# Kernel tuning notes

Hardware: AMD Instinct MI355X
Metric: run time of the kernel (lower is better)

The kernel has to match this reference:

```python
import jax, jax.numpy as jnp
import numpy as np

N_NODES = 1_000_000
HID = 64
BATCH = 262_144


def _gru_cell(x, h, w_ih, w_hh, b_ih, b_hh):
    # PyTorch GRUCell semantics. w_ih/w_hh: [3H, H]; gate order r, z, n.
    gi = x @ w_ih.T + b_ih
    gh = h @ w_hh.T + b_hh
    i_r, i_z, i_n = jnp.split(gi, 3, axis=-1)
    h_r, h_z, h_n = jnp.split(gh, 3, axis=-1)
    r = jax.nn.sigmoid(i_r + h_r)
    z = jax.nn.sigmoid(i_z + h_z)
    n = jnp.tanh(i_n + r * h_n)
    return (1.0 - z) * n + z * h


def setup_inputs() -> dict:
    key = jax.random.key(0)
    ks = jax.random.split(key, 16)
    H = HID
    s = lambda fan_in: 1.0 / np.sqrt(fan_in)
    return {
        "node_pairs": jax.random.randint(ks[0], (BATCH, 2), 0, N_NODES, dtype=jnp.int64)
        if jax.config.jax_enable_x64 else jax.random.randint(ks[0], (BATCH, 2), 0, N_NODES, dtype=jnp.int32),
        "memory": jax.random.normal(ks[1], (N_NODES, H), dtype=jnp.float32),
        "msg_w1": jax.random.uniform(ks[2], (H, 2 * H), jnp.float32, -s(2 * H), s(2 * H)),
        "msg_b1": jax.random.uniform(ks[3], (H,), jnp.float32, -s(2 * H), s(2 * H)),
        "msg_w2": jax.random.uniform(ks[4], (H, H), jnp.float32, -s(H), s(H)),
        "msg_b2": jax.random.uniform(ks[5], (H,), jnp.float32, -s(H), s(H)),
        "gru_w_ih": jax.random.uniform(ks[6], (3 * H, H), jnp.float32, -s(H), s(H)),
        "gru_w_hh": jax.random.uniform(ks[7], (3 * H, H), jnp.float32, -s(H), s(H)),
        "gru_b_ih": jax.random.uniform(ks[8], (3 * H,), jnp.float32, -s(H), s(H)),
        "gru_b_hh": jax.random.uniform(ks[9], (3 * H,), jnp.float32, -s(H), s(H)),
        "lp_w1": jax.random.uniform(ks[10], (H, 2 * H), jnp.float32, -s(2 * H), s(2 * H)),
        "lp_b1": jax.random.uniform(ks[11], (H,), jnp.float32, -s(2 * H), s(2 * H)),
        "lp_w2": jax.random.uniform(ks[12], (1, H), jnp.float32, -s(H), s(H)),
        "lp_b2": jax.random.uniform(ks[13], (1,), jnp.float32, -s(H), s(H)),
    }


def reference(node_pairs, memory, msg_w1, msg_b1, msg_w2, msg_b2,
              gru_w_ih, gru_w_hh, gru_b_ih, gru_b_hh,
              lp_w1, lp_b1, lp_w2, lp_b2):
    n1_mem = memory[node_pairs[:, 0]]  # [B, H]
    n2_mem = memory[node_pairs[:, 1]]  # [B, H]
    x = jnp.concatenate([n1_mem, n2_mem], axis=1)  # [B, 2H]
    messages = jax.nn.relu(x @ msg_w1.T + msg_b1) @ msg_w2.T + msg_b2  # [B, H]
    n1_upd = _gru_cell(messages, n1_mem, gru_w_ih, gru_w_hh, gru_b_ih, gru_b_hh)
    n2_upd = _gru_cell(messages, n2_mem, gru_w_ih, gru_w_hh, gru_b_ih, gru_b_hh)
    combined = jnp.concatenate([n1_upd, n2_upd], axis=1)  # [B, 2H]
    h = jax.nn.relu(combined @ lp_w1.T + lp_b1)  # dropout inactive in eval
    out = jax.nn.sigmoid(h @ lp_w2.T + lp_b2)  # [B, 1]
    return out.squeeze(-1)
```

## Files before the change

### kernel.cpp

```cpp
#include <hip/hip_runtime.h>

#define BATCH 262144

typedef __attribute__((ext_vector_type(8))) short short8;
typedef __attribute__((ext_vector_type(4))) float f32x4;

static __device__ __forceinline__ unsigned cvtpk(float lo, float hi) {
    unsigned r;
    asm("v_cvt_pk_bf16_f32 %0, %1, %2" : "=v"(r) : "v"(lo), "v"(hi));
    return r;
}
static __device__ __forceinline__ float b2f(short s) {
    return __uint_as_float(((unsigned)(unsigned short)s) << 16);
}
static __device__ __forceinline__ float sigm(float x) { return 1.0f / (1.0f + __expf(-x)); }
static __device__ __forceinline__ float tanh_f(float x) { return 1.0f - 2.0f / (__expf(2.0f * x) + 1.0f); }

#define WAVE_FENCE() asm volatile("" ::: "memory")

static __device__ __forceinline__ int sw128(int row, int cb) { return row * 128 + (cb ^ ((row & 7) << 4)); }
static __device__ __forceinline__ int sw256(int row, int cb) { return row * 256 + (cb ^ ((row & 7) << 4)); }

#define WLDS_BYTES 90112
#define NCHUNK (WLDS_BYTES / 16)

__global__ __launch_bounds__(768) void tgn_kernel(
    const int* __restrict__ pairs, const float* __restrict__ memory,
    const float* __restrict__ w1g, const float* __restrict__ w2g,
    const float* __restrict__ wihg, const float* __restrict__ whhg,
    const float* __restrict__ lw1g,
    const float* __restrict__ b1, const float* __restrict__ b2,
    const float* __restrict__ bih, const float* __restrict__ bhh,
    const float* __restrict__ lb1, const float* __restrict__ lw2,
    const float* __restrict__ lb2, float* __restrict__ out)
{
    __shared__ __align__(16) char wlds[WLDS_BYTES];
    __shared__ __align__(16) char work[12][6144];

    const int tid = threadIdx.x;
    const int w  = tid >> 6;
    const int l  = tid & 63;
    const int lr = l & 15;
    const int lg = l >> 4;

    for (int c = tid; c < NCHUNK; c += 768) {
        int byte = c * 16;
        int e    = c * 8;
        const float* src;
        int base, sh;
        if (e < 8192)       { src = w1g  + e;         base = 0;     sh = 8; }
        else if (e < 12288) { src = w2g  + e - 8192;  base = 16384; sh = 7; }
        else if (e < 24576) { src = wihg + e - 12288; base = 24576; sh = 7; }
        else if (e < 36864) { src = whhg + e - 24576; base = 49152; sh = 7; }
        else                { src = lw1g + e - 36864; base = 73728; sh = 8; }
        f32x4 v0 = *(const f32x4*)src;
        f32x4 v1 = *(const f32x4*)(src + 4);
        union { unsigned u[4]; short8 s; } r;
        r.u[0] = cvtpk(v0[0], v0[1]); r.u[1] = cvtpk(v0[2], v0[3]);
        r.u[2] = cvtpk(v1[0], v1[1]); r.u[3] = cvtpk(v1[2], v1[3]);
        int t   = byte - base;
        int row = t >> sh;
        int dst = base + (t ^ ((row & 7) << 4));
        *(short8*)(wlds + dst) = r.s;
    }
    __syncthreads();

    char* n1b = &work[w][0];
    char* n2b = &work[w][2048];
    char* hmb = &work[w][4096];

    const char* w1l  = wlds + 0;
    const char* w2l  = wlds + 16384;
    const char* wihl = wlds + 24576;
    const char* whhl = wlds + 49152;
    const char* lw1l = wlds + 73728;

    const f32x4 z4 = {0.0f, 0.0f, 0.0f, 0.0f};

    const int waveid = blockIdx.x * 12 + w;

    int2 pr[4];
#pragma unroll
    for (int rr = 0; rr < 4; ++rr)
        pr[rr] = *(const int2*)(pairs + (waveid * 16 + rr * 4 + lg) * 2);

#pragma unroll 1
    for (int tile = waveid; tile < 16384; tile += 3072) {
        const int r0 = tile * 16;

#pragma unroll
        for (int rr = 0; rr < 4; ++rr) {
            int row = rr * 4 + lg;
            f32x4 v1 = *(const f32x4*)(memory + (long)pr[rr].x * 64 + lr * 4);
            f32x4 v2 = *(const f32x4*)(memory + (long)pr[rr].y * 64 + lr * 4);
            uint2 c1v, c2v;
            c1v.x = cvtpk(v1[0], v1[1]); c1v.y = cvtpk(v1[2], v1[3]);
            c2v.x = cvtpk(v2[0], v2[1]); c2v.y = cvtpk(v2[2], v2[3]);
            int off = sw128(row, lr * 8);
            *(uint2*)(n1b + off) = c1v;
            *(uint2*)(n2b + off) = c2v;
        }
        {
            int next = tile + 3072;
            if (next < 16384) {
#pragma unroll
                for (int rr = 0; rr < 4; ++rr)
                    pr[rr] = *(const int2*)(pairs + (next * 16 + rr * 4 + lg) * 2);
            }
        }
        WAVE_FENCE();

        f32x4 acc[4];
#pragma unroll
        for (int nt = 0; nt < 4; ++nt) acc[nt] = z4;
#pragma unroll
        for (int kt = 0; kt < 4; ++kt) {
            const char* base = (kt < 2) ? n1b : n2b;
            short8 a = *(const short8*)(base + sw128(lr, (kt & 1) * 64 + lg * 16));
#pragma unroll
            for (int nt = 0; nt < 4; ++nt) {
                short8 b = *(const short8*)(w1l + sw256(nt * 16 + lr, kt * 64 + lg * 16));
                acc[nt] = __builtin_amdgcn_mfma_f32_16x16x32_bf16(a, b, acc[nt], 0, 0, 0);
            }
        }
#pragma unroll
        for (int nt = 0; nt < 4; ++nt) {
            float bv = b1[nt * 16 + lr];
            unsigned p01 = cvtpk(fmaxf(acc[nt][0] + bv, 0.0f), fmaxf(acc[nt][1] + bv, 0.0f));
            unsigned p23 = cvtpk(fmaxf(acc[nt][2] + bv, 0.0f), fmaxf(acc[nt][3] + bv, 0.0f));
            int cb = nt * 32 + lr * 2;
            *(short*)(hmb + sw128(lg * 4 + 0, cb)) = (short)p01;
            *(short*)(hmb + sw128(lg * 4 + 1, cb)) = (short)(p01 >> 16);
            *(short*)(hmb + sw128(lg * 4 + 2, cb)) = (short)p23;
            *(short*)(hmb + sw128(lg * 4 + 3, cb)) = (short)(p23 >> 16);
        }
        WAVE_FENCE();

#pragma unroll
        for (int nt = 0; nt < 4; ++nt) acc[nt] = z4;
#pragma unroll
        for (int kt = 0; kt < 2; ++kt) {
            short8 a = *(const short8*)(hmb + sw128(lr, kt * 64 + lg * 16));
#pragma unroll
            for (int nt = 0; nt < 4; ++nt) {
                short8 b = *(const short8*)(w2l + sw128(nt * 16 + lr, kt * 64 + lg * 16));
                acc[nt] = __builtin_amdgcn_mfma_f32_16x16x32_bf16(a, b, acc[nt], 0, 0, 0);
            }
        }
#pragma unroll
        for (int nt = 0; nt < 4; ++nt) {
            float bv = b2[nt * 16 + lr];
            unsigned p01 = cvtpk(acc[nt][0] + bv, acc[nt][1] + bv);
            unsigned p23 = cvtpk(acc[nt][2] + bv, acc[nt][3] + bv);
            int cb = nt * 32 + lr * 2;
            *(short*)(hmb + sw128(lg * 4 + 0, cb)) = (short)p01;
            *(short*)(hmb + sw128(lg * 4 + 1, cb)) = (short)(p01 >> 16);
            *(short*)(hmb + sw128(lg * 4 + 2, cb)) = (short)p23;
            *(short*)(hmb + sw128(lg * 4 + 3, cb)) = (short)(p23 >> 16);
        }
        WAVE_FENCE();

        short8 am[2], a1[2], a2[2];
#pragma unroll
        for (int kt = 0; kt < 2; ++kt) {
            am[kt] = *(const short8*)(hmb + sw128(lr, kt * 64 + lg * 16));
            a1[kt] = *(const short8*)(n1b + sw128(lr, kt * 64 + lg * 16));
            a2[kt] = *(const short8*)(n2b + sw128(lr, kt * 64 + lg * 16));
        }
#pragma unroll
        for (int nt = 0; nt < 4; ++nt) {
            f32x4 gir = z4, giz = z4, gin = z4;
            f32x4 g1r = z4, g1z = z4, g1n = z4;
            f32x4 g2r = z4, g2z = z4, g2n = z4;
#pragma unroll
            for (int kt = 0; kt < 2; ++kt) {
                int ko = kt * 64 + lg * 16;
                short8 bir = *(const short8*)(wihl + sw128((0 + nt) * 16 + lr, ko));
                short8 biz = *(const short8*)(wihl + sw128((4 + nt) * 16 + lr, ko));
                short8 bin = *(const short8*)(wihl + sw128((8 + nt) * 16 + lr, ko));
                short8 bhr = *(const short8*)(whhl + sw128((0 + nt) * 16 + lr, ko));
                short8 bhz = *(const short8*)(whhl + sw128((4 + nt) * 16 + lr, ko));
                short8 bhn = *(const short8*)(whhl + sw128((8 + nt) * 16 + lr, ko));
                gir = __builtin_amdgcn_mfma_f32_16x16x32_bf16(am[kt], bir, gir, 0, 0, 0);
                giz = __builtin_amdgcn_mfma_f32_16x16x32_bf16(am[kt], biz, giz, 0, 0, 0);
                gin = __builtin_amdgcn_mfma_f32_16x16x32_bf16(am[kt], bin, gin, 0, 0, 0);
                g1r = __builtin_amdgcn_mfma_f32_16x16x32_bf16(a1[kt], bhr, g1r, 0, 0, 0);
                g1z = __builtin_amdgcn_mfma_f32_16x16x32_bf16(a1[kt], bhz, g1z, 0, 0, 0);
                g1n = __builtin_amdgcn_mfma_f32_16x16x32_bf16(a1[kt], bhn, g1n, 0, 0, 0);
                g2r = __builtin_amdgcn_mfma_f32_16x16x32_bf16(a2[kt], bhr, g2r, 0, 0, 0);
                g2z = __builtin_amdgcn_mfma_f32_16x16x32_bf16(a2[kt], bhz, g2z, 0, 0, 0);
                g2n = __builtin_amdgcn_mfma_f32_16x16x32_bf16(a2[kt], bhn, g2n, 0, 0, 0);
            }
            int j = nt * 16 + lr;
            float bir_ = bih[j], biz_ = bih[64 + j], bin_ = bih[128 + j];
            float bhr_ = bhh[j], bhz_ = bhh[64 + j], bhn_ = bhh[128 + j];
            float o1[4], o2[4];
#pragma unroll
            for (int r = 0; r < 4; ++r) {
                int row = lg * 4 + r;
                float i_r = gir[r] + bir_;
                float i_z = giz[r] + biz_;
                float i_n = gin[r] + bin_;
                float rg = sigm(i_r + g1r[r] + bhr_);
                float zg = sigm(i_z + g1z[r] + bhz_);
                float ng = tanh_f(i_n + rg * (g1n[r] + bhn_));
                float h  = b2f(*(const short*)(n1b + sw128(row, j * 2)));
                o1[r] = (1.0f - zg) * ng + zg * h;
                rg = sigm(i_r + g2r[r] + bhr_);
                zg = sigm(i_z + g2z[r] + bhz_);
                ng = tanh_f(i_n + rg * (g2n[r] + bhn_));
                h  = b2f(*(const short*)(n2b + sw128(row, j * 2)));
                o2[r] = (1.0f - zg) * ng + zg * h;
            }
            unsigned q01 = cvtpk(o1[0], o1[1]), q23 = cvtpk(o1[2], o1[3]);
            unsigned s01 = cvtpk(o2[0], o2[1]), s23 = cvtpk(o2[2], o2[3]);
            *(short*)(n1b + sw128(lg * 4 + 0, j * 2)) = (short)q01;
            *(short*)(n1b + sw128(lg * 4 + 1, j * 2)) = (short)(q01 >> 16);
            *(short*)(n1b + sw128(lg * 4 + 2, j * 2)) = (short)q23;
            *(short*)(n1b + sw128(lg * 4 + 3, j * 2)) = (short)(q23 >> 16);
            *(short*)(n2b + sw128(lg * 4 + 0, j * 2)) = (short)s01;
            *(short*)(n2b + sw128(lg * 4 + 1, j * 2)) = (short)(s01 >> 16);
            *(short*)(n2b + sw128(lg * 4 + 2, j * 2)) = (short)s23;
            *(short*)(n2b + sw128(lg * 4 + 3, j * 2)) = (short)(s23 >> 16);
        }
        WAVE_FENCE();

        f32x4 acc5[4];
#pragma unroll
        for (int nt = 0; nt < 4; ++nt) acc5[nt] = z4;
#pragma unroll
        for (int kt = 0; kt < 4; ++kt) {
            const char* base = (kt < 2) ? n1b : n2b;
            short8 a = *(const short8*)(base + sw128(lr, (kt & 1) * 64 + lg * 16));
#pragma unroll
            for (int nt = 0; nt < 4; ++nt) {
                short8 b = *(const short8*)(lw1l + sw256(nt * 16 + lr, kt * 64 + lg * 16));
                acc5[nt] = __builtin_amdgcn_mfma_f32_16x16x32_bf16(a, b, acc5[nt], 0, 0, 0);
            }
        }

        float part[4] = {0.0f, 0.0f, 0.0f, 0.0f};
#pragma unroll
        for (int nt = 0; nt < 4; ++nt) {
            float w2v = lw2[nt * 16 + lr];
            float bv  = lb1[nt * 16 + lr];
#pragma unroll
            for (int r = 0; r < 4; ++r)
                part[r] += fmaxf(acc5[nt][r] + bv, 0.0f) * w2v;
        }
        float lb2v = lb2[0];
#pragma unroll
        for (int r = 0; r < 4; ++r) {
            float p = part[r];
            p += __shfl_xor(p, 1);
            p += __shfl_xor(p, 2);
            p += __shfl_xor(p, 4);
            p += __shfl_xor(p, 8);
            if (lr == 0) out[r0 + lg * 4 + r] = sigm(p + lb2v);
        }
    }
}

extern "C" void kernel_launch(void* const* d_in, const int* in_sizes, int n_in,
                              void* d_out, int out_size, void* d_ws, size_t ws_size,
                              hipStream_t stream) {
    const int*   pairs  = (const int*)d_in[0];
    const float* memory = (const float*)d_in[1];
    const float* w1  = (const float*)d_in[2];
    const float* b1  = (const float*)d_in[3];
    const float* w2  = (const float*)d_in[4];
    const float* b2  = (const float*)d_in[5];
    const float* wih = (const float*)d_in[6];
    const float* whh = (const float*)d_in[7];
    const float* bih = (const float*)d_in[8];
    const float* bhh = (const float*)d_in[9];
    const float* lw1 = (const float*)d_in[10];
    const float* lb1 = (const float*)d_in[11];
    const float* lw2 = (const float*)d_in[12];
    const float* lb2 = (const float*)d_in[13];

    tgn_kernel<<<256, 768, 0, stream>>>(pairs, memory, w1, w2, wih, whh, lw1,
                                        b1, b2, bih, bhh, lb1, lw2, lb2,
                                        (float*)d_out);
}
```

Before: 105.5 us.

## Process two 16-row tiles per wave to reuse weight fragments across MFMAs

Each wave now handles two independent 16-row tiles (A and B) per iteration, with 6 waves per block instead of 12. Every weight fragment loaded from LDS feeds two MFMAs instead of one, which halves weight LDS traffic per row and gives independent MFMA chains for ILP. The cost is fewer resident waves per CU and higher register pressure (double accumulators), which reduces latency hiding for the random memory gathers.

```diff
diff --git a/kernel.cpp b/kernel.cpp
--- a/kernel.cpp
+++ b/kernel.cpp
@@ -24,7 +24,7 @@
 #define WLDS_BYTES 90112
 #define NCHUNK (WLDS_BYTES / 16)
 
-__global__ __launch_bounds__(768) void tgn_kernel(
+__global__ __launch_bounds__(384) void tgn_kernel(
     const int* __restrict__ pairs, const float* __restrict__ memory,
     const float* __restrict__ w1g, const float* __restrict__ w2g,
     const float* __restrict__ wihg, const float* __restrict__ whhg,
@@ -35,7 +35,7 @@
     const float* __restrict__ lb2, float* __restrict__ out)
 {
     __shared__ __align__(16) char wlds[WLDS_BYTES];
-    __shared__ __align__(16) char work[12][6144];
+    __shared__ __align__(16) char work[6][12288];
 
     const int tid = threadIdx.x;
     const int w  = tid >> 6;
@@ -43,7 +43,7 @@
     const int lr = l & 15;
     const int lg = l >> 4;
 
-    for (int c = tid; c < NCHUNK; c += 768) {
+    for (int c = tid; c < NCHUNK; c += 384) {
         int byte = c * 16;
         int e    = c * 8;
         const float* src;
@@ -65,9 +65,12 @@
     }
     __syncthreads();
 
-    char* n1b = &work[w][0];
-    char* n2b = &work[w][2048];
-    char* hmb = &work[w][4096];
+    char* n1A = &work[w][0];
+    char* n2A = &work[w][2048];
+    char* hmA = &work[w][4096];
+    char* n1B = &work[w][6144];
+    char* n2B = &work[w][8192];
+    char* hmB = &work[w][10240];
 
     const char* w1l  = wlds + 0;
     const char* w2l  = wlds + 16384;
@@ -77,101 +80,137 @@
 
     const f32x4 z4 = {0.0f, 0.0f, 0.0f, 0.0f};
 
-    const int waveid = blockIdx.x * 12 + w;
-
-    int2 pr[4];
-#pragma unroll
-    for (int rr = 0; rr < 4; ++rr)
-        pr[rr] = *(const int2*)(pairs + (waveid * 16 + rr * 4 + lg) * 2);
+    const int stid = blockIdx.x * 6 + w;
+
+    int2 prA[4], prB[4];
+#pragma unroll
+    for (int rr = 0; rr < 4; ++rr) {
+        prA[rr] = *(const int2*)(pairs + (stid * 32 + rr * 4 + lg) * 2);
+        prB[rr] = *(const int2*)(pairs + (stid * 32 + 16 + rr * 4 + lg) * 2);
+    }
 
 #pragma unroll 1
-    for (int tile = waveid; tile < 16384; tile += 3072) {
-        const int r0 = tile * 16;
+    for (int st = stid; st < 8192; st += 1536) {
+        const int r0 = st * 32;
 
 #pragma unroll
         for (int rr = 0; rr < 4; ++rr) {
             int row = rr * 4 + lg;
-            f32x4 v1 = *(const f32x4*)(memory + (long)pr[rr].x * 64 + lr * 4);
-            f32x4 v2 = *(const f32x4*)(memory + (long)pr[rr].y * 64 + lr * 4);
-            uint2 c1v, c2v;
-            c1v.x = cvtpk(v1[0], v1[1]); c1v.y = cvtpk(v1[2], v1[3]);
-            c2v.x = cvtpk(v2[0], v2[1]); c2v.y = cvtpk(v2[2], v2[3]);
+            f32x4 vA1 = *(const f32x4*)(memory + (long)prA[rr].x * 64 + lr * 4);
+            f32x4 vA2 = *(const f32x4*)(memory + (long)prA[rr].y * 64 + lr * 4);
+            f32x4 vB1 = *(const f32x4*)(memory + (long)prB[rr].x * 64 + lr * 4);
+            f32x4 vB2 = *(const f32x4*)(memory + (long)prB[rr].y * 64 + lr * 4);
+            uint2 cA1, cA2, cB1, cB2;
+            cA1.x = cvtpk(vA1[0], vA1[1]); cA1.y = cvtpk(vA1[2], vA1[3]);
+            cA2.x = cvtpk(vA2[0], vA2[1]); cA2.y = cvtpk(vA2[2], vA2[3]);
+            cB1.x = cvtpk(vB1[0], vB1[1]); cB1.y = cvtpk(vB1[2], vB1[3]);
+            cB2.x = cvtpk(vB2[0], vB2[1]); cB2.y = cvtpk(vB2[2], vB2[3]);
             int off = sw128(row, lr * 8);
-            *(uint2*)(n1b + off) = c1v;
-            *(uint2*)(n2b + off) = c2v;
+            *(uint2*)(n1A + off) = cA1;
+            *(uint2*)(n2A + off) = cA2;
+            *(uint2*)(n1B + off) = cB1;
+            *(uint2*)(n2B + off) = cB2;
         }
         {
-            int next = tile + 3072;
-            if (next < 16384) {
-#pragma unroll
-                for (int rr = 0; rr < 4; ++rr)
-                    pr[rr] = *(const int2*)(pairs + (next * 16 + rr * 4 + lg) * 2);
+            int next = st + 1536;
+            if (next < 8192) {
+#pragma unroll
+                for (int rr = 0; rr < 4; ++rr) {
+                    prA[rr] = *(const int2*)(pairs + (next * 32 + rr * 4 + lg) * 2);
+                    prB[rr] = *(const int2*)(pairs + (next * 32 + 16 + rr * 4 + lg) * 2);
+                }
             }
         }
         WAVE_FENCE();
 
-        f32x4 acc[4];
-#pragma unroll
-        for (int nt = 0; nt < 4; ++nt) acc[nt] = z4;
+        f32x4 accA[4], accB[4];
+#pragma unroll
+        for (int nt = 0; nt < 4; ++nt) { accA[nt] = z4; accB[nt] = z4; }
 #pragma unroll
         for (int kt = 0; kt < 4; ++kt) {
-            const char* base = (kt < 2) ? n1b : n2b;
-            short8 a = *(const short8*)(base + sw128(lr, (kt & 1) * 64 + lg * 16));
+            const char* baA = (kt < 2) ? n1A : n2A;
+            const char* baB = (kt < 2) ? n1B : n2B;
+            int ao = sw128(lr, (kt & 1) * 64 + lg * 16);
+            short8 aA = *(const short8*)(baA + ao);
+            short8 aB = *(const short8*)(baB + ao);
 #pragma unroll
             for (int nt = 0; nt < 4; ++nt) {
                 short8 b = *(const short8*)(w1l + sw256(nt * 16 + lr, kt * 64 + lg * 16));
-                acc[nt] = __builtin_amdgcn_mfma_f32_16x16x32_bf16(a, b, acc[nt], 0, 0, 0);
+                accA[nt] = __builtin_amdgcn_mfma_f32_16x16x32_bf16(aA, b, accA[nt], 0, 0, 0);
+                accB[nt] = __builtin_amdgcn_mfma_f32_16x16x32_bf16(aB, b, accB[nt], 0, 0, 0);
             }
         }
 #pragma unroll
         for (int nt = 0; nt < 4; ++nt) {
             float bv = b1[nt * 16 + lr];
-            unsigned p01 = cvtpk(fmaxf(acc[nt][0] + bv, 0.0f), fmaxf(acc[nt][1] + bv, 0.0f));
-            unsigned p23 = cvtpk(fmaxf(acc[nt][2] + bv, 0.0f), fmaxf(acc[nt][3] + bv, 0.0f));
+            unsigned a01 = cvtpk(fmaxf(accA[nt][0] + bv, 0.0f), fmaxf(accA[nt][1] + bv, 0.0f));
+            unsigned a23 = cvtpk(fmaxf(accA[nt][2] + bv, 0.0f), fmaxf(accA[nt][3] + bv, 0.0f));
+            unsigned b01 = cvtpk(fmaxf(accB[nt][0] + bv, 0.0f), fmaxf(accB[nt][1] + bv, 0.0f));
+            unsigned b23 = cvtpk(fmaxf(accB[nt][2] + bv, 0.0f), fmaxf(accB[nt][3] + bv, 0.0f));
             int cb = nt * 32 + lr * 2;
-            *(short*)(hmb + sw128(lg * 4 + 0, cb)) = (short)p01;
-            *(short*)(hmb + sw128(lg * 4 + 1, cb)) = (short)(p01 >> 16);
-            *(short*)(hmb + sw128(lg * 4 + 2, cb)) = (short)p23;
-            *(short*)(hmb + sw128(lg * 4 + 3, cb)) = (short)(p23 >> 16);
+            *(short*)(hmA + sw128(lg * 4 + 0, cb)) = (short)a01;
+            *(short*)(hmA + sw128(lg * 4 + 1, cb)) = (short)(a01 >> 16);
+            *(short*)(hmA + sw128(lg * 4 + 2, cb)) = (short)a23;
+            *(short*)(hmA + sw128(lg * 4 + 3, cb)) = (short)(a23 >> 16);
+            *(short*)(hmB + sw128(lg * 4 + 0, cb)) = (short)b01;
+            *(short*)(hmB + sw128(lg * 4 + 1, cb)) = (short)(b01 >> 16);
+            *(short*)(hmB + sw128(lg * 4 + 2, cb)) = (short)b23;
+            *(short*)(hmB + sw128(lg * 4 + 3, cb)) = (short)(b23 >> 16);
         }
         WAVE_FENCE();
 
 #pragma unroll
-        for (int nt = 0; nt < 4; ++nt) acc[nt] = z4;
+        for (int nt = 0; nt < 4; ++nt) { accA[nt] = z4; accB[nt] = z4; }
 #pragma unroll
         for (int kt = 0; kt < 2; ++kt) {
-            short8 a = *(const short8*)(hmb + sw128(lr, kt * 64 + lg * 16));
+            int ao = sw128(lr, kt * 64 + lg * 16);
+            short8 aA = *(const short8*)(hmA + ao);
+            short8 aB = *(const short8*)(hmB + ao);
 #pragma unroll
             for (int nt = 0; nt < 4; ++nt) {
                 short8 b = *(const short8*)(w2l + sw128(nt * 16 + lr, kt * 64 + lg * 16));
-                acc[nt] = __builtin_amdgcn_mfma_f32_16x16x32_bf16(a, b, acc[nt], 0, 0, 0);
+                accA[nt] = __builtin_amdgcn_mfma_f32_16x16x32_bf16(aA, b, accA[nt], 0, 0, 0);
+                accB[nt] = __builtin_amdgcn_mfma_f32_16x16x32_bf16(aB, b, accB[nt], 0, 0, 0);
             }
         }
 #pragma unroll
         for (int nt = 0; nt < 4; ++nt) {
             float bv = b2[nt * 16 + lr];
-            unsigned p01 = cvtpk(acc[nt][0] + bv, acc[nt][1] + bv);
-            unsigned p23 = cvtpk(acc[nt][2] + bv, acc[nt][3] + bv);
+            unsigned a01 = cvtpk(accA[nt][0] + bv, accA[nt][1] + bv);
+            unsigned a23 = cvtpk(accA[nt][2] + bv, accA[nt][3] + bv);
+            unsigned b01 = cvtpk(accB[nt][0] + bv, accB[nt][1] + bv);
+            unsigned b23 = cvtpk(accB[nt][2] + bv, accB[nt][3] + bv);
             int cb = nt * 32 + lr * 2;
-            *(short*)(hmb + sw128(lg * 4 + 0, cb)) = (short)p01;
-            *(short*)(hmb + sw128(lg * 4 + 1, cb)) = (short)(p01 >> 16);
-            *(short*)(hmb + sw128(lg * 4 + 2, cb)) = (short)p23;
-            *(short*)(hmb + sw128(lg * 4 + 3, cb)) = (short)(p23 >> 16);
+            *(short*)(hmA + sw128(lg * 4 + 0, cb)) = (short)a01;
+            *(short*)(hmA + sw128(lg * 4 + 1, cb)) = (short)(a01 >> 16);
+            *(short*)(hmA + sw128(lg * 4 + 2, cb)) = (short)a23;
+            *(short*)(hmA + sw128(lg * 4 + 3, cb)) = (short)(a23 >> 16);
+            *(short*)(hmB + sw128(lg * 4 + 0, cb)) = (short)b01;
+            *(short*)(hmB + sw128(lg * 4 + 1, cb)) = (short)(b01 >> 16);
+            *(short*)(hmB + sw128(lg * 4 + 2, cb)) = (short)b23;
+            *(short*)(hmB + sw128(lg * 4 + 3, cb)) = (short)(b23 >> 16);
         }
         WAVE_FENCE();
 
-        short8 am[2], a1[2], a2[2];
+        short8 amA[2], amB[2], a1A[2], a1B[2], a2A[2], a2B[2];
 #pragma unroll
         for (int kt = 0; kt < 2; ++kt) {
-            am[kt] = *(const short8*)(hmb + sw128(lr, kt * 64 + lg * 16));
-            a1[kt] = *(const short8*)(n1b + sw128(lr, kt * 64 + lg * 16));
-            a2[kt] = *(const short8*)(n2b + sw128(lr, kt * 64 + lg * 16));
+            int ao = sw128(lr, kt * 64 + lg * 16);
+            amA[kt] = *(const short8*)(hmA + ao);
+            amB[kt] = *(const short8*)(hmB + ao);
+            a1A[kt] = *(const short8*)(n1A + ao);
+            a1B[kt] = *(const short8*)(n1B + ao);
+            a2A[kt] = *(const short8*)(n2A + ao);
+            a2B[kt] = *(const short8*)(n2B + ao);
         }
 #pragma unroll
         for (int nt = 0; nt < 4; ++nt) {
-            f32x4 gir = z4, giz = z4, gin = z4;
-            f32x4 g1r = z4, g1z = z4, g1n = z4;
-            f32x4 g2r = z4, g2z = z4, g2n = z4;
+            f32x4 girA = z4, gizA = z4, ginA = z4;
+            f32x4 g1rA = z4, g1zA = z4, g1nA = z4;
+            f32x4 g2rA = z4, g2zA = z4, g2nA = z4;
+            f32x4 girB = z4, gizB = z4, ginB = z4;
+            f32x4 g1rB = z4, g1zB = z4, g1nB = z4;
+            f32x4 g2rB = z4, g2zB = z4, g2nB = z4;
 #pragma unroll
             for (int kt = 0; kt < 2; ++kt) {
                 int ko = kt * 64 + lg * 16;
@@ -181,82 +220,133 @@
                 short8 bhr = *(const short8*)(whhl + sw128((0 + nt) * 16 + lr, ko));
                 short8 bhz = *(const short8*)(whhl + sw128((4 + nt) * 16 + lr, ko));
                 short8 bhn = *(const short8*)(whhl + sw128((8 + nt) * 16 + lr, ko));
-                gir = __builtin_amdgcn_mfma_f32_16x16x32_bf16(am[kt], bir, gir, 0, 0, 0);
-                giz = __builtin_amdgcn_mfma_f32_16x16x32_bf16(am[kt], biz, giz, 0, 0, 0);
-                gin = __builtin_amdgcn_mfma_f32_16x16x32_bf16(am[kt], bin, gin, 0, 0, 0);
-                g1r = __builtin_amdgcn_mfma_f32_16x16x32_bf16(a1[kt], bhr, g1r, 0, 0, 0);
-                g1z = __builtin_amdgcn_mfma_f32_16x16x32_bf16(a1[kt], bhz, g1z, 0, 0, 0);
-                g1n = __builtin_amdgcn_mfma_f32_16x16x32_bf16(a1[kt], bhn, g1n, 0, 0, 0);
-                g2r = __builtin_amdgcn_mfma_f32_16x16x32_bf16(a2[kt], bhr, g2r, 0, 0, 0);
-                g2z = __builtin_amdgcn_mfma_f32_16x16x32_bf16(a2[kt], bhz, g2z, 0, 0, 0);
-                g2n = __builtin_amdgcn_mfma_f32_16x16x32_bf16(a2[kt], bhn, g2n, 0, 0, 0);
+                girA = __builtin_amdgcn_mfma_f32_16x16x32_bf16(amA[kt], bir, girA, 0, 0, 0);
+                girB = __builtin_amdgcn_mfma_f32_16x16x32_bf16(amB[kt], bir, girB, 0, 0, 0);
+                gizA = __builtin_amdgcn_mfma_f32_16x16x32_bf16(amA[kt], biz, gizA, 0, 0, 0);
+                gizB = __builtin_amdgcn_mfma_f32_16x16x32_bf16(amB[kt], biz, gizB, 0, 0, 0);
+                ginA = __builtin_amdgcn_mfma_f32_16x16x32_bf16(amA[kt], bin, ginA, 0, 0, 0);
+                ginB = __builtin_amdgcn_mfma_f32_16x16x32_bf16(amB[kt], bin, ginB, 0, 0, 0);
+                g1rA = __builtin_amdgcn_mfma_f32_16x16x32_bf16(a1A[kt], bhr, g1rA, 0, 0, 0);
+                g1rB = __builtin_amdgcn_mfma_f32_16x16x32_bf16(a1B[kt], bhr, g1rB, 0, 0, 0);
+                g1zA = __builtin_amdgcn_mfma_f32_16x16x32_bf16(a1A[kt], bhz, g1zA, 0, 0, 0);
+                g1zB = __builtin_amdgcn_mfma_f32_16x16x32_bf16(a1B[kt], bhz, g1zB, 0, 0, 0);
+                g1nA = __builtin_amdgcn_mfma_f32_16x16x32_bf16(a1A[kt], bhn, g1nA, 0, 0, 0);
+                g1nB = __builtin_amdgcn_mfma_f32_16x16x32_bf16(a1B[kt], bhn, g1nB, 0, 0, 0);
+                g2rA = __builtin_amdgcn_mfma_f32_16x16x32_bf16(a2A[kt], bhr, g2rA, 0, 0, 0);
+                g2rB = __builtin_amdgcn_mfma_f32_16x16x32_bf16(a2B[kt], bhr, g2rB, 0, 0, 0);
+                g2zA = __builtin_amdgcn_mfma_f32_16x16x32_bf16(a2A[kt], bhz, g2zA, 0, 0, 0);
+                g2zB = __builtin_amdgcn_mfma_f32_16x16x32_bf16(a2B[kt], bhz, g2zB, 0, 0, 0);
+                g2nA = __builtin_amdgcn_mfma_f32_16x16x32_bf16(a2A[kt], bhn, g2nA, 0, 0, 0);
+                g2nB = __builtin_amdgcn_mfma_f32_16x16x32_bf16(a2B[kt], bhn, g2nB, 0, 0, 0);
             }
             int j = nt * 16 + lr;
             float bir_ = bih[j], biz_ = bih[64 + j], bin_ = bih[128 + j];
             float bhr_ = bhh[j], bhz_ = bhh[64 + j], bhn_ = bhh[128 + j];
-            float o1[4], o2[4];
-#pragma unroll
-            for (int r = 0; r < 4; ++r) {
-                int row = lg * 4 + r;
-                float i_r = gir[r] + bir_;
-                float i_z = giz[r] + biz_;
-                float i_n = gin[r] + bin_;
-                float rg = sigm(i_r + g1r[r] + bhr_);
-                float zg = sigm(i_z + g1z[r] + bhz_);
-                float ng = tanh_f(i_n + rg * (g1n[r] + bhn_));
-                float h  = b2f(*(const short*)(n1b + sw128(row, j * 2)));
-                o1[r] = (1.0f - zg) * ng + zg * h;
-                rg = sigm(i_r + g2r[r] + bhr_);
-                zg = sigm(i_z + g2z[r] + bhz_);
-                ng = tanh_f(i_n + rg * (g2n[r] + bhn_));
-                h  = b2f(*(const short*)(n2b + sw128(row, j * 2)));
-                o2[r] = (1.0f - zg) * ng + zg * h;
-            }
-            unsigned q01 = cvtpk(o1[0], o1[1]), q23 = cvtpk(o1[2], o1[3]);
-            unsigned s01 = cvtpk(o2[0], o2[1]), s23 = cvtpk(o2[2], o2[3]);
-            *(short*)(n1b + sw128(lg * 4 + 0, j * 2)) = (short)q01;
-            *(short*)(n1b + sw128(lg * 4 + 1, j * 2)) = (short)(q01 >> 16);
-            *(short*)(n1b + sw128(lg * 4 + 2, j * 2)) = (short)q23;
-            *(short*)(n1b + sw128(lg * 4 + 3, j * 2)) = (short)(q23 >> 16);
-            *(short*)(n2b + sw128(lg * 4 + 0, j * 2)) = (short)s01;
-            *(short*)(n2b + sw128(lg * 4 + 1, j * 2)) = (short)(s01 >> 16);
-            *(short*)(n2b + sw128(lg * 4 + 2, j * 2)) = (short)s23;
-            *(short*)(n2b + sw128(lg * 4 + 3, j * 2)) = (short)(s23 >> 16);
+            {
+                float o1[4], o2[4];
+#pragma unroll
+                for (int r = 0; r < 4; ++r) {
+                    int row = lg * 4 + r;
+                    float i_r = girA[r] + bir_;
+                    float i_z = gizA[r] + biz_;
+                    float i_n = ginA[r] + bin_;
+                    float rg = sigm(i_r + g1rA[r] + bhr_);
+                    float zg = sigm(i_z + g1zA[r] + bhz_);
+                    float ng = tanh_f(i_n + rg * (g1nA[r] + bhn_));
+                    float h  = b2f(*(const short*)(n1A + sw128(row, j * 2)));
+                    o1[r] = (1.0f - zg) * ng + zg * h;
+                    rg = sigm(i_r + g2rA[r] + bhr_);
+                    zg = sigm(i_z + g2zA[r] + bhz_);
+                    ng = tanh_f(i_n + rg * (g2nA[r] + bhn_));
+                    h  = b2f(*(const short*)(n2A + sw128(row, j * 2)));
+                    o2[r] = (1.0f - zg) * ng + zg * h;
+                }
+                unsigned q01 = cvtpk(o1[0], o1[1]), q23 = cvtpk(o1[2], o1[3]);
+                unsigned s01 = cvtpk(o2[0], o2[1]), s23 = cvtpk(o2[2], o2[3]);
+                *(short*)(n1A + sw128(lg * 4 + 0, j * 2)) = (short)q01;
+                *(short*)(n1A + sw128(lg * 4 + 1, j * 2)) = (short)(q01 >> 16);
+                *(short*)(n1A + sw128(lg * 4 + 2, j * 2)) = (short)q23;
+                *(short*)(n1A + sw128(lg * 4 + 3, j * 2)) = (short)(q23 >> 16);
+                *(short*)(n2A + sw128(lg * 4 + 0, j * 2)) = (short)s01;
+                *(short*)(n2A + sw128(lg * 4 + 1, j * 2)) = (short)(s01 >> 16);
+                *(short*)(n2A + sw128(lg * 4 + 2, j * 2)) = (short)s23;
+                *(short*)(n2A + sw128(lg * 4 + 3, j * 2)) = (short)(s23 >> 16);
+            }
+            {
+                float o1[4], o2[4];
+#pragma unroll
+                for (int r = 0; r < 4; ++r) {
+                    int row = lg * 4 + r;
+                    float i_r = girB[r] + bir_;
+                    float i_z = gizB[r] + biz_;
+                    float i_n = ginB[r] + bin_;
+                    float rg = sigm(i_r + g1rB[r] + bhr_);
+                    float zg = sigm(i_z + g1zB[r] + bhz_);
+                    float ng = tanh_f(i_n + rg * (g1nB[r] + bhn_));
+                    float h  = b2f(*(const short*)(n1B + sw128(row, j * 2)));
+                    o1[r] = (1.0f - zg) * ng + zg * h;
+                    rg = sigm(i_r + g2rB[r] + bhr_);
+                    zg = sigm(i_z + g2zB[r] + bhz_);
+                    ng = tanh_f(i_n + rg * (g2nB[r] + bhn_));
+                    h  = b2f(*(const short*)(n2B + sw128(row, j * 2)));
+                    o2[r] = (1.0f - zg) * ng + zg * h;
+                }
+                unsigned q01 = cvtpk(o1[0], o1[1]), q23 = cvtpk(o1[2], o1[3]);
+                unsigned s01 = cvtpk(o2[0], o2[1]), s23 = cvtpk(o2[2], o2[3]);
+                *(short*)(n1B + sw128(lg * 4 + 0, j * 2)) = (short)q01;
+                *(short*)(n1B + sw128(lg * 4 + 1, j * 2)) = (short)(q01 >> 16);
+                *(short*)(n1B + sw128(lg * 4 + 2, j * 2)) = (short)q23;
+                *(short*)(n1B + sw128(lg * 4 + 3, j * 2)) = (short)(q23 >> 16);
+                *(short*)(n2B + sw128(lg * 4 + 0, j * 2)) = (short)s01;
+                *(short*)(n2B + sw128(lg * 4 + 1, j * 2)) = (short)(s01 >> 16);
+                *(short*)(n2B + sw128(lg * 4 + 2, j * 2)) = (short)s23;
+                *(short*)(n2B + sw128(lg * 4 + 3, j * 2)) = (short)(s23 >> 16);
+            }
         }
         WAVE_FENCE();
 
-        f32x4 acc5[4];
-#pragma unroll
-        for (int nt = 0; nt < 4; ++nt) acc5[nt] = z4;
+        f32x4 acc5A[4], acc5B[4];
+#pragma unroll
+        for (int nt = 0; nt < 4; ++nt) { acc5A[nt] = z4; acc5B[nt] = z4; }
 #pragma unroll
         for (int kt = 0; kt < 4; ++kt) {
-            const char* base = (kt < 2) ? n1b : n2b;
-            short8 a = *(const short8*)(base + sw128(lr, (kt & 1) * 64 + lg * 16));
+            const char* baA = (kt < 2) ? n1A : n2A;
+            const char* baB = (kt < 2) ? n1B : n2B;
+            int ao = sw128(lr, (kt & 1) * 64 + lg * 16);
+            short8 aA = *(const short8*)(baA + ao);
+            short8 aB = *(const short8*)(baB + ao);
 #pragma unroll
             for (int nt = 0; nt < 4; ++nt) {
                 short8 b = *(const short8*)(lw1l + sw256(nt * 16 + lr, kt * 64 + lg * 16));
-                acc5[nt] = __builtin_amdgcn_mfma_f32_16x16x32_bf16(a, b, acc5[nt], 0, 0, 0);
-            }
-        }
-
-        float part[4] = {0.0f, 0.0f, 0.0f, 0.0f};
+                acc5A[nt] = __builtin_amdgcn_mfma_f32_16x16x32_bf16(aA, b, acc5A[nt], 0, 0, 0);
+                acc5B[nt] = __builtin_amdgcn_mfma_f32_16x16x32_bf16(aB, b, acc5B[nt], 0, 0, 0);
+            }
+        }
+
+        float partA[4] = {0.0f, 0.0f, 0.0f, 0.0f};
+        float partB[4] = {0.0f, 0.0f, 0.0f, 0.0f};
 #pragma unroll
         for (int nt = 0; nt < 4; ++nt) {
             float w2v = lw2[nt * 16 + lr];
             float bv  = lb1[nt * 16 + lr];
 #pragma unroll
-            for (int r = 0; r < 4; ++r)
-                part[r] += fmaxf(acc5[nt][r] + bv, 0.0f) * w2v;
+            for (int r = 0; r < 4; ++r) {
+                partA[r] += fmaxf(acc5A[nt][r] + bv, 0.0f) * w2v;
+                partB[r] += fmaxf(acc5B[nt][r] + bv, 0.0f) * w2v;
+            }
         }
         float lb2v = lb2[0];
 #pragma unroll
         for (int r = 0; r < 4; ++r) {
-            float p = part[r];
-            p += __shfl_xor(p, 1);
-            p += __shfl_xor(p, 2);
-            p += __shfl_xor(p, 4);
-            p += __shfl_xor(p, 8);
-            if (lr == 0) out[r0 + lg * 4 + r] = sigm(p + lb2v);
+            float pA = partA[r], pB = partB[r];
+            pA += __shfl_xor(pA, 1); pB += __shfl_xor(pB, 1);
+            pA += __shfl_xor(pA, 2); pB += __shfl_xor(pB, 2);
+            pA += __shfl_xor(pA, 4); pB += __shfl_xor(pB, 4);
+            pA += __shfl_xor(pA, 8); pB += __shfl_xor(pB, 8);
+            if (lr == 0) {
+                out[r0 + lg * 4 + r]      = sigm(pA + lb2v);
+                out[r0 + 16 + lg * 4 + r] = sigm(pB + lb2v);
+            }
         }
     }
 }
@@ -279,7 +369,7 @@
     const float* lw2 = (const float*)d_in[12];
     const float* lb2 = (const float*)d_in[13];
 
-    tgn_kernel<<<256, 768, 0, stream>>>(pairs, memory, w1, w2, wih, whh, lw1,
+    tgn_kernel<<<256, 384, 0, stream>>>(pairs, memory, w1, w2, wih, whh, lw1,
                                         b1, b2, bih, bhh, lb1, lw2, lb2,
                                         (float*)d_out);
 }
```

New measurement: 135.4 us. +28.4%, slower.
